# Optimization experiments

Measured on AMD Instinct MI355X. Metric: run time of the kernel, lower is better.

Reference implementation:

```python
import jax, jax.numpy as jnp
import numpy as np

N = 4096      # sentences in document
K = 32        # clusters (args.k)
D = 256       # input_dim
H = 128       # hidden_dim
P_SAL = 0.5   # args.percent_sal


def setup_inputs() -> dict:
    key = jax.random.key(0)
    ks = jax.random.split(key, 12)
    s = 1.0 / np.sqrt(H)
    inp = {
        "sent_gae_embeds": jax.random.normal(ks[0], (N, D), jnp.float32),
        "labels": jax.random.randint(ks[1], (N,), 0, K),
        # GRU layer 0 (torch gate order r,z,n)
        "W_ih0": jax.random.uniform(ks[2], (3 * H, D), jnp.float32, -s, s),
        "W_hh0": jax.random.uniform(ks[3], (3 * H, H), jnp.float32, -s, s),
        "b_ih0": jax.random.uniform(ks[4], (3 * H,), jnp.float32, -s, s),
        "b_hh0": jax.random.uniform(ks[5], (3 * H,), jnp.float32, -s, s),
        # GRU layer 1
        "W_ih1": jax.random.uniform(ks[6], (3 * H, H), jnp.float32, -s, s),
        "W_hh1": jax.random.uniform(ks[7], (3 * H, H), jnp.float32, -s, s),
        "b_ih1": jax.random.uniform(ks[8], (3 * H,), jnp.float32, -s, s),
        "b_hh1": jax.random.uniform(ks[9], (3 * H,), jnp.float32, -s, s),
        # weight-normed linear: W = g * v / ||v|| (norm over input dim)
        "lin_v": jax.random.normal(ks[10], (1, D + H), jnp.float32) * 0.05,
        "lin_g": jnp.ones((1, 1), jnp.float32),
        "lin_b": jnp.zeros((1,), jnp.float32),
    }
    return inp


def _gru_layer(x, W_ih, W_hh, b_ih, b_hh):
    # x: [T, B, Din] -> outputs [T, B, H]
    xw = jnp.einsum("tbd,gd->tbg", x, W_ih) + b_ih  # precompute input gates

    def step(h, xw_t):
        hw = h @ W_hh.T + b_hh
        r = jax.nn.sigmoid(xw_t[:, :H] + hw[:, :H])
        z = jax.nn.sigmoid(xw_t[:, H:2 * H] + hw[:, H:2 * H])
        n = jnp.tanh(xw_t[:, 2 * H:] + r * hw[:, 2 * H:])
        h_new = (1.0 - z) * n + z * h
        return h_new, h_new

    h0 = jnp.zeros((x.shape[1], H), x.dtype)
    _, outs = jax.lax.scan(step, h0, xw)
    return outs


def reference(sent_gae_embeds, labels, W_ih0, W_hh0, b_ih0, b_hh0,
              W_ih1, W_hh1, b_ih1, b_hh1, lin_v, lin_g, lin_b):
    # --- cluster gather: position of each sentence within its cluster ---
    onehot = jax.nn.one_hot(labels, K, dtype=jnp.int32)          # [N, K]
    pos = jnp.cumsum(onehot, axis=0)[jnp.arange(N), labels] - 1  # [N]
    lengths = onehot.sum(axis=0)                                 # [K]

    # padded per-cluster sequences: [T=N, B=K, D]
    padded = jnp.zeros((N, K, D), sent_gae_embeds.dtype).at[pos, labels].set(sent_gae_embeds)

    # --- 2-layer GRU over each cluster sequence ---
    h1 = _gru_layer(padded, W_ih0, W_hh0, b_ih0, b_hh0)
    h2 = _gru_layer(h1, W_ih1, W_hh1, b_ih1, b_hh1)
    len_c = jnp.maximum(lengths, 1)  # empty cluster -> length-1 zero sequence
    cluster_embeds = h2[len_c - 1, jnp.arange(K)]  # [K, H]

    # --- scatter cluster embeds back onto sentences (sent detached as in torch) ---
    sent_d = jax.lax.stop_gradient(sent_gae_embeds)
    final_embeds = jnp.concatenate([sent_d, cluster_embeds[labels]], axis=-1)  # [N, D+H]

    # weight-normed linear + tanh
    Wn = lin_g * lin_v / jnp.linalg.norm(lin_v, axis=1, keepdims=True)
    scores = jnp.tanh(final_embeds @ Wn.T + lin_b)[:, 0]  # [N]

    # salience: per-cluster segment-sum normalization
    clu_scores = jax.ops.segment_sum(scores, labels, num_segments=K)
    sal_scores = scores / clu_scores[labels]

    # position scores: max(0.5, exp(-(i+1)/n**(1/3)))
    inv = np.float32(1.0 / (N ** (1.0 / 3.0)))
    pos_scores = jnp.maximum(0.5, jnp.exp(-(jnp.arange(N, dtype=jnp.float32) + 1.0) * inv))

    return P_SAL * sal_scores + (1.0 - P_SAL) * pos_scores
```

## Files before the change

### kernel.cpp

```cpp
#include <hip/hip_runtime.h>
#include <cmath>

#define NN 4096
#define KK 32
#define DD 256
#define HH 128
#define G3 384
#define CH 16
#define RH 136

typedef __attribute__((ext_vector_type(8))) _Float16 h8;
typedef __attribute__((ext_vector_type(4))) float f32x4;

__global__ __launch_bounds__(1024) void setup_k(
    const int* __restrict__ labels, const float* __restrict__ lin_v,
    const float* __restrict__ lin_g,
    const float* __restrict__ Whh0, const float* __restrict__ Wih1,
    const float* __restrict__ Whh1,
    int* __restrict__ order, int* __restrict__ pos, int* __restrict__ len,
    int* __restrict__ starts, float* __restrict__ scale,
    _Float16* __restrict__ P) {
  if (blockIdx.x != 0) {
    const int gid = (int)(blockIdx.x - 1) * 1024 + threadIdx.x;
    if (gid >= 18432) return;
    const int lane = gid & 63;
    const int kt = (gid >> 6) & 3;
    const int nt = (gid >> 8) % 24;
    const int mat = (gid >> 8) / 24;
    const float* W = (mat == 0) ? Whh0 : (mat == 1 ? Wih1 : Whh1);
    const int n = nt * 16 + (lane & 15);
    const int kbase = kt * 32 + (lane >> 4) * 8;
    _Float16* dst = P + (size_t)gid * 8;
#pragma unroll
    for (int j = 0; j < 8; ++j) dst[j] = (_Float16)W[(size_t)n * HH + kbase + j];
    return;
  }
  const int t = threadIdx.x;
  const int wv = t >> 6, lane = t & 63;
  __shared__ int lens_s[KK];
  for (int cc = 0; cc < 2; ++cc) {
    const int c = wv * 2 + cc;
    int count = 0;
    for (int base = 0; base < NN; base += 64) {
      const int i = base + lane;
      const bool f = (labels[i] == c);
      const unsigned long long m = __ballot(f);
      if (f) {
        const int p = count + __popcll(m & ((1ull << lane) - 1ull));
        order[c * NN + p] = i;
        pos[i] = p;
      }
      count += __popcll(m);
    }
    if (lane == 0) { lens_s[c] = count; len[c] = count; }
  }
  __syncthreads();
  if (wv == 0) {
    int lm = 0;
    if (lane < KK) { const int l = lens_s[lane]; lm = (l > 0) ? l : 1; }
    int inc = lm;
    for (int off = 1; off < KK; off <<= 1) {
      const int o = __shfl_up(inc, off);
      if (lane >= off) inc += o;
    }
    if (lane < KK) starts[lane] = inc - lm;
    if (lane == KK - 1) starts[KK] = inc;
  } else if (wv == 1) {
    float s = 0.f;
    for (int j = lane; j < G3; j += 64) { const float v = lin_v[j]; s += v * v; }
    for (int off = 32; off; off >>= 1) s += __shfl_down(s, off);
    if (lane == 0) scale[0] = lin_g[0] / sqrtf(s);
  }
}

__global__ __launch_bounds__(256) void gemm_ih_k(
    const float* __restrict__ X, const float* __restrict__ W,
    const float* __restrict__ bias,
    const int* __restrict__ labels, const int* __restrict__ pos,
    const int* __restrict__ starts, float* __restrict__ out) {
  __shared__ float Xs[16][132];
  __shared__ float Ws[16][68];
  const int i0 = blockIdx.x * 128;
  const int g0 = blockIdx.y * 64;
  const int t  = threadIdx.x;
  const int it = t & 15;
  const int gt = t >> 4;
  float acc[8][4] = {};
  for (int k0 = 0; k0 < DD; k0 += 16) {
#pragma unroll
    for (int l = 0; l < 2; ++l) {
      const int u = t * 2 + l;
      const int r = u >> 2;
      const int cq = u & 3;
      const float4 f = *(const float4*)(X + (size_t)(i0 + r) * DD + k0 + cq * 4);
      Xs[cq * 4 + 0][r] = f.x; Xs[cq * 4 + 1][r] = f.y;
      Xs[cq * 4 + 2][r] = f.z; Xs[cq * 4 + 3][r] = f.w;
    }
    {
      const int r = t >> 2;
      const int cq = t & 3;
      const float4 f = *(const float4*)(W + (size_t)(g0 + r) * DD + k0 + cq * 4);
      Ws[cq * 4 + 0][r] = f.x; Ws[cq * 4 + 1][r] = f.y;
      Ws[cq * 4 + 2][r] = f.z; Ws[cq * 4 + 3][r] = f.w;
    }
    __syncthreads();
#pragma unroll
    for (int k = 0; k < 16; ++k) {
      float a[8], b[4];
#pragma unroll
      for (int x = 0; x < 8; ++x) a[x] = Xs[k][it * 8 + x];
#pragma unroll
      for (int y = 0; y < 4; ++y) b[y] = Ws[k][gt * 4 + y];
#pragma unroll
      for (int x = 0; x < 8; ++x)
#pragma unroll
        for (int y = 0; y < 4; ++y)
          acc[x][y] += a[x] * b[y];
    }
    __syncthreads();
  }
  const float4 bs = *(const float4*)(bias + g0 + gt * 4);
#pragma unroll
  for (int x = 0; x < 8; ++x) {
    const int gi = i0 + it * 8 + x;
    const int slot = starts[labels[gi]] + pos[gi];
    float4 o;
    o.x = acc[x][0] + bs.x; o.y = acc[x][1] + bs.y;
    o.z = acc[x][2] + bs.z; o.w = acc[x][3] + bs.w;
    *(float4*)(out + (size_t)slot * G3 + g0 + gt * 4) = o;
  }
}

__global__ __launch_bounds__(768) void gru_fused_k(
    const float* __restrict__ xw0,
    const _Float16* __restrict__ pack,
    const float* __restrict__ b_hh0, const float* __restrict__ b_ih0,
    const float* __restrict__ b_ih1, const float* __restrict__ b_hh1,
    const int* __restrict__ starts, const int* __restrict__ len,
    const int* __restrict__ order, const float* __restrict__ sent,
    const float* __restrict__ lin_v, const float* __restrict__ scale,
    const float* __restrict__ lin_b, float* __restrict__ out) {
  const int c = blockIdx.x;
  const int t = threadIdx.x;
  const int wv = t >> 6, lane = t & 63;
  const int group = wv >> 2;
  const int v = wv & 3;
  h8 B[6][4];
  {
    const _Float16* mp = pack + (size_t)group * (24 * 4 * 64 * 8);
#pragma unroll
    for (int i = 0; i < 6; ++i) {
      const int nt = (i >> 1) * 8 + 2 * v + (i & 1);
#pragma unroll
      for (int kt = 0; kt < 4; ++kt)
        B[i][kt] = *(const h8*)(mp + ((size_t)(nt * 4 + kt) * 64 + lane) * 8);
    }
  }
  const int L = len[c], start = starts[c];
  const int Lr = (L > 0) ? L : 1;
  const bool use_bih0 = (L == 0);
  __shared__ __align__(16) float xwbuf[2 * CH * G3];
  __shared__ __align__(16) _Float16 ring[16][2 * RH];
  __shared__ __align__(16) _Float16 hp2[2][2][HH];
  __shared__ float xw1buf[2][8][G3];
  __shared__ float ce_s[HH];
  __shared__ float vbuf[G3];
  __shared__ float sc_s[2048];
  __shared__ float sc_red;
  {
    _Float16* rp = &ring[0][0];
    for (int u = t; u < 16 * 2 * RH; u += 768) rp[u] = (_Float16)0.f;
  }
  if (t < HH) {
    hp2[0][0][t] = (_Float16)0.f; hp2[0][1][t] = (_Float16)0.f;
    hp2[1][0][t] = (_Float16)0.f; hp2[1][1][t] = (_Float16)0.f;
  }
  if (!use_bih0) {
    const float4* src = (const float4*)(xw0 + (size_t)start * G3);
    float4* dst = (float4*)xwbuf;
    dst[t] = src[t];
    dst[t + 768] = src[t + 768];
  }
  const int tg = 32 * v + (lane & 31);
  float bhr = 0.f, bhz = 0.f, bhn = 0.f;
  float bir = 0.f, biz = 0.f, bin = 0.f;
  float h = 0.f;
  if (lane < 32) {
    if (group == 0) {
      bhr = b_hh0[tg]; bhz = b_hh0[HH + tg]; bhn = b_hh0[2 * HH + tg];
      if (use_bih0) {
        bir = b_ih0[tg]; biz = b_ih0[HH + tg]; bin = b_ih0[2 * HH + tg];
      }
    } else if (group == 2) {
      bhr = b_hh1[tg]; bhz = b_hh1[HH + tg]; bhn = b_hh1[2 * HH + tg];
      bir = b_ih1[tg]; biz = b_ih1[HH + tg]; bin = b_ih1[2 * HH + tg];
    }
  }
  __syncthreads();
  const int q = lane >> 4;
  const int row = lane & 15;
  const int hs = (row == 0 || row == 4) ? 0 : 1;
  const bool hiacc = ((lane >> 4) & 1) != 0;
  for (int it2 = 0; it2 < Lr + 9; ++it2) {
    const int par = it2 & 1;
    if (!use_bih0 && (it2 & (CH - 1)) == 0 && it2 + CH < Lr) {
      const float4* src = (const float4*)(xw0 + (size_t)(start + it2 + CH) * G3);
      float4* dst = (float4*)(xwbuf + ((((it2 >> 4) + 1) & 1) ? CH * G3 : 0));
      dst[t] = src[t];
      dst[t + 768] = src[t + 768];
    }
    if (group == 0) {
      if (it2 < Lr) {
        float xr = bir, xz = biz, xn = bin;
        if (!use_bih0 && lane < 32) {
          const float* xrow = xwbuf + ((it2 >> 4) & 1) * (CH * G3)
                                    + (it2 & (CH - 1)) * G3;
          xr = xrow[tg]; xz = xrow[HH + tg]; xn = xrow[2 * HH + tg];
        }
        const _Float16* abse = &ring[(it2 - 1) & 15][hs * RH];
        h8 A[4];
#pragma unroll
        for (int kt = 0; kt < 4; ++kt)
          A[kt] = *(const h8*)(abse + kt * 32 + q * 8);
        f32x4 a0[6];
#pragma unroll
        for (int i = 0; i < 6; ++i) {
          f32x4 a = {0.f, 0.f, 0.f, 0.f};
#pragma unroll
          for (int kt = 0; kt < 4; ++kt)
            a = __builtin_amdgcn_mfma_f32_16x16x32_f16(A[kt], B[i][kt], a, 0, 0, 0);
          a0[i] = a;
        }
        if (lane < 32) {
          const float hwrA = a0[0][0] + a0[0][1], hwrB = a0[1][0] + a0[1][1];
          const float hwzA = a0[2][0] + a0[2][1], hwzB = a0[3][0] + a0[3][1];
          const float hwnA = a0[4][0] + a0[4][1], hwnB = a0[5][0] + a0[5][1];
          const float hwr = hiacc ? hwrB : hwrA;
          const float hwz = hiacc ? hwzB : hwzA;
          const float hwn = hiacc ? hwnB : hwnA;
          const float r = 1.f / (1.f + __expf(-(xr + bhr + hwr)));
          const float z = 1.f / (1.f + __expf(-(xz + bhz + hwz)));
          float tgt = xn + r * (bhn + hwn);
          tgt = fminf(fmaxf(tgt, -15.f), 15.f);
          const float e = __expf(2.f * tgt);
          const float n = (e - 1.f) / (e + 1.f);
          h = (1.f - z) * n + z * h;
          const _Float16 hi = (_Float16)h;
          _Float16* rs = &ring[it2 & 15][0];
          rs[tg] = hi;  rs[RH + tg] = (_Float16)(h - (float)hi);
        }
      }
    } else if (group == 1) {
      if (it2 >= 8 && (it2 & 7) == 0 && it2 - 8 < Lr) {
        const int c8 = it2 - 8;
        const int m = lane & 15;
        const int s = m >> 1, half = m & 1;
        const _Float16* abse = &ring[(c8 + s) & 15][half * RH];
        h8 A[4];
#pragma unroll
        for (int kt = 0; kt < 4; ++kt)
          A[kt] = *(const h8*)(abse + kt * 32 + q * 8);
        const int cbuf = (c8 >> 3) & 1;
        float* xo0 = &xw1buf[cbuf][2 * q][0];
        float* xo1 = &xw1buf[cbuf][2 * q + 1][0];
#pragma unroll
        for (int i = 0; i < 6; ++i) {
          f32x4 a = {0.f, 0.f, 0.f, 0.f};
#pragma unroll
          for (int kt = 0; kt < 4; ++kt)
            a = __builtin_amdgcn_mfma_f32_16x16x32_f16(A[kt], B[i][kt], a, 0, 0, 0);
          const int nt = (i >> 1) * 8 + 2 * v + (i & 1);
          const int col = nt * 16 + (lane & 15);
          xo0[col] = a[0] + a[1];
          xo1[col] = a[2] + a[3];
        }
      }
    } else {
      if (it2 >= 9) {
        const int j = it2 - 9;
        float xr = 0.f, xz = 0.f, xn = 0.f;
        if (lane < 32) {
          const float* xi = xw1buf[(j >> 3) & 1][j & 7];
          xr = xi[tg] + bir; xz = xi[HH + tg] + biz; xn = xi[2 * HH + tg] + bin;
        }
        const _Float16* hbase = hp2[par][hs];
        h8 A[4];
#pragma unroll
        for (int kt = 0; kt < 4; ++kt)
          A[kt] = *(const h8*)(hbase + kt * 32 + q * 8);
        f32x4 a1[6];
#pragma unroll
        for (int i = 0; i < 6; ++i) {
          f32x4 a = {0.f, 0.f, 0.f, 0.f};
#pragma unroll
          for (int kt = 0; kt < 4; ++kt)
            a = __builtin_amdgcn_mfma_f32_16x16x32_f16(A[kt], B[i][kt], a, 0, 0, 0);
          a1[i] = a;
        }
        if (lane < 32) {
          const float hwrA = a1[0][0] + a1[0][1], hwrB = a1[1][0] + a1[1][1];
          const float hwzA = a1[2][0] + a1[2][1], hwzB = a1[3][0] + a1[3][1];
          const float hwnA = a1[4][0] + a1[4][1], hwnB = a1[5][0] + a1[5][1];
          const float hwr = hiacc ? hwrB : hwrA;
          const float hwz = hiacc ? hwzB : hwzA;
          const float hwn = hiacc ? hwnB : hwnA;
          const float r = 1.f / (1.f + __expf(-(xr + bhr + hwr)));
          const float z = 1.f / (1.f + __expf(-(xz + bhz + hwz)));
          float tgt = xn + r * (bhn + hwn);
          tgt = fminf(fmaxf(tgt, -15.f), 15.f);
          const float e = __expf(2.f * tgt);
          const float n = (e - 1.f) / (e + 1.f);
          h = (1.f - z) * n + z * h;
          const _Float16 hi = (_Float16)h;
          hp2[par ^ 1][0][tg] = hi;
          hp2[par ^ 1][1][tg] = (_Float16)(h - (float)hi);
        }
      }
    }
    __syncthreads();
  }
  if (L == 0) return;
  if (group == 2 && lane < 32) ce_s[tg] = h;
  if (t < G3) vbuf[t] = lin_v[t];
  __syncthreads();
  if (wv == 0) {
    float cd = ce_s[lane] * vbuf[DD + lane] + ce_s[64 + lane] * vbuf[DD + 64 + lane];
    for (int off = 32; off; off >>= 1) cd += __shfl_down(cd, off);
    if (lane == 0) sc_red = cd;
  }
  __syncthreads();
  const float cedot = sc_red;
  const float sc = scale[0], lb = lin_b[0];
  const int Lc = (L < 2048) ? L : 2048;
  for (int p = wv; p < Lc; p += 12) {
    const int i = order[c * NN + p];
    const float4 a = *(const float4*)(sent + (size_t)i * DD + lane * 4);
    const float4 b = ((const float4*)vbuf)[lane];
    float d = a.x * b.x + a.y * b.y + a.z * b.z + a.w * b.w;
    for (int off = 32; off; off >>= 1) d += __shfl_down(d, off);
    if (lane == 0) sc_s[p] = tanhf(sc * (d + cedot) + lb);
  }
  __syncthreads();
  if (wv == 0) {
    float s = 0.f;
    for (int p = lane; p < Lc; p += 64) s += sc_s[p];
    for (int off = 32; off; off >>= 1) s += __shfl_down(s, off);
    if (lane == 0) sc_red = 1.f / s;
  }
  __syncthreads();
  const float inv = sc_red;
  for (int p = t; p < Lc; p += 768) {
    const int i = order[c * NN + p];
    float ps = __expf(-(float)(i + 1) * 0.0625f);
    ps = fmaxf(0.5f, ps);
    out[i] = 0.5f * (sc_s[p] * inv) + 0.5f * ps;
  }
}

extern "C" void kernel_launch(void* const* d_in, const int* in_sizes, int n_in,
                              void* d_out, int out_size, void* d_ws, size_t ws_size,
                              hipStream_t stream) {
  const float* sent   = (const float*)d_in[0];
  const int*   labels = (const int*)d_in[1];
  const float* W_ih0  = (const float*)d_in[2];
  const float* W_hh0  = (const float*)d_in[3];
  const float* b_ih0  = (const float*)d_in[4];
  const float* b_hh0  = (const float*)d_in[5];
  const float* W_ih1  = (const float*)d_in[6];
  const float* W_hh1  = (const float*)d_in[7];
  const float* b_ih1  = (const float*)d_in[8];
  const float* b_hh1  = (const float*)d_in[9];
  const float* lin_v  = (const float*)d_in[10];
  const float* lin_g  = (const float*)d_in[11];
  const float* lin_b  = (const float*)d_in[12];
  float* out = (float*)d_out;

  char* ws = (char*)d_ws;
  size_t off = 0;
  auto alloc = [&](size_t bytes) -> void* {
    void* p = ws + off;
    off = (off + bytes + 255) & ~(size_t)255;
    return p;
  };
  int*   order  = (int*)  alloc((size_t)KK * NN * sizeof(int));
  int*   pos    = (int*)  alloc(NN * sizeof(int));
  int*   len    = (int*)  alloc(KK * sizeof(int));
  int*   starts = (int*)  alloc((KK + 1) * sizeof(int));
  float* scale  = (float*)alloc(sizeof(float));
  _Float16* pack = (_Float16*)alloc((size_t)18432 * 8 * sizeof(_Float16));
  float* xw     = (float*)alloc((size_t)(NN + KK + 2 * CH) * G3 * sizeof(float));
  (void)ws_size; (void)in_sizes; (void)n_in; (void)out_size;

  setup_k<<<dim3(19), dim3(1024), 0, stream>>>(
      labels, lin_v, lin_g, W_hh0, W_ih1, W_hh1,
      order, pos, len, starts, scale, pack);
  gemm_ih_k<<<dim3(32, 6), dim3(256), 0, stream>>>(
      sent, W_ih0, b_ih0, labels, pos, starts, xw);
  gru_fused_k<<<dim3(KK), dim3(768), 0, stream>>>(
      xw, pack, b_hh0, b_ih0, b_ih1, b_hh1, starts, len,
      order, sent, lin_v, scale, lin_b, out);
}
```

Baseline: 277.9 us.

## Merge setup and input-GEMM kernels, gather xw rows by order in GRU kernel

Folds the label bucketing, weight packing, norm scale and input-gate GEMM into one launch. The GEMM no longer depends on the per-cluster prefix sums, so it writes rows in sentence order, and the GRU kernel gathers each cluster's rows through the order index when refilling its shared buffer. This removes a kernel launch and the serial dependency on the starts/pos computation. In exchange, the GRU prefetch now does scattered, index-dependent row loads instead of contiguous ones.

```diff
diff --git a/kernel.cpp b/kernel.cpp
--- a/kernel.cpp
+++ b/kernel.cpp
@@ -12,17 +12,19 @@
 typedef __attribute__((ext_vector_type(8))) _Float16 h8;
 typedef __attribute__((ext_vector_type(4))) float f32x4;
 
-__global__ __launch_bounds__(1024) void setup_k(
+__global__ __launch_bounds__(256) void prep_k(
     const int* __restrict__ labels, const float* __restrict__ lin_v,
     const float* __restrict__ lin_g,
     const float* __restrict__ Whh0, const float* __restrict__ Wih1,
     const float* __restrict__ Whh1,
-    int* __restrict__ order, int* __restrict__ pos, int* __restrict__ len,
-    int* __restrict__ starts, float* __restrict__ scale,
-    _Float16* __restrict__ P) {
-  if (blockIdx.x != 0) {
-    const int gid = (int)(blockIdx.x - 1) * 1024 + threadIdx.x;
-    if (gid >= 18432) return;
+    const float* __restrict__ sent, const float* __restrict__ W_ih0,
+    const float* __restrict__ b_ih0,
+    int* __restrict__ order, int* __restrict__ len, float* __restrict__ scale,
+    _Float16* __restrict__ P, float* __restrict__ xw) {
+  const int blk = blockIdx.x;
+  const int t = threadIdx.x;
+  if (blk < 72) {
+    const int gid = blk * 256 + t;
     const int lane = gid & 63;
     const int kt = (gid >> 6) & 3;
     const int nt = (gid >> 8) % 24;
@@ -35,54 +37,34 @@
     for (int j = 0; j < 8; ++j) dst[j] = (_Float16)W[(size_t)n * HH + kbase + j];
     return;
   }
-  const int t = threadIdx.x;
-  const int wv = t >> 6, lane = t & 63;
-  __shared__ int lens_s[KK];
-  for (int cc = 0; cc < 2; ++cc) {
-    const int c = wv * 2 + cc;
+  if (blk < 80) {
+    const int wv = t >> 6, lane = t & 63;
+    const int c = (blk - 72) * 4 + wv;
     int count = 0;
     for (int base = 0; base < NN; base += 64) {
       const int i = base + lane;
       const bool f = (labels[i] == c);
       const unsigned long long m = __ballot(f);
-      if (f) {
-        const int p = count + __popcll(m & ((1ull << lane) - 1ull));
-        order[c * NN + p] = i;
-        pos[i] = p;
-      }
+      if (f) order[c * NN + count + __popcll(m & ((1ull << lane) - 1ull))] = i;
       count += __popcll(m);
     }
-    if (lane == 0) { lens_s[c] = count; len[c] = count; }
-  }
-  __syncthreads();
-  if (wv == 0) {
-    int lm = 0;
-    if (lane < KK) { const int l = lens_s[lane]; lm = (l > 0) ? l : 1; }
-    int inc = lm;
-    for (int off = 1; off < KK; off <<= 1) {
-      const int o = __shfl_up(inc, off);
-      if (lane >= off) inc += o;
-    }
-    if (lane < KK) starts[lane] = inc - lm;
-    if (lane == KK - 1) starts[KK] = inc;
-  } else if (wv == 1) {
-    float s = 0.f;
-    for (int j = lane; j < G3; j += 64) { const float v = lin_v[j]; s += v * v; }
-    for (int off = 32; off; off >>= 1) s += __shfl_down(s, off);
-    if (lane == 0) scale[0] = lin_g[0] / sqrtf(s);
-  }
-}
-
-__global__ __launch_bounds__(256) void gemm_ih_k(
-    const float* __restrict__ X, const float* __restrict__ W,
-    const float* __restrict__ bias,
-    const int* __restrict__ labels, const int* __restrict__ pos,
-    const int* __restrict__ starts, float* __restrict__ out) {
+    if (lane == 0) len[c] = count;
+    return;
+  }
+  if (blk == 80) {
+    if (t < 64) {
+      float s = 0.f;
+      for (int j = t; j < G3; j += 64) { const float v = lin_v[j]; s += v * v; }
+      for (int off = 32; off; off >>= 1) s += __shfl_down(s, off);
+      if (t == 0) scale[0] = lin_g[0] / sqrtf(s);
+    }
+    return;
+  }
   __shared__ float Xs[16][132];
   __shared__ float Ws[16][68];
-  const int i0 = blockIdx.x * 128;
-  const int g0 = blockIdx.y * 64;
-  const int t  = threadIdx.x;
+  const int g = blk - 81;
+  const int i0 = (g & 31) * 128;
+  const int g0 = (g >> 5) * 64;
   const int it = t & 15;
   const int gt = t >> 4;
   float acc[8][4] = {};
@@ -92,14 +74,14 @@
       const int u = t * 2 + l;
       const int r = u >> 2;
       const int cq = u & 3;
-      const float4 f = *(const float4*)(X + (size_t)(i0 + r) * DD + k0 + cq * 4);
+      const float4 f = *(const float4*)(sent + (size_t)(i0 + r) * DD + k0 + cq * 4);
       Xs[cq * 4 + 0][r] = f.x; Xs[cq * 4 + 1][r] = f.y;
       Xs[cq * 4 + 2][r] = f.z; Xs[cq * 4 + 3][r] = f.w;
     }
     {
       const int r = t >> 2;
       const int cq = t & 3;
-      const float4 f = *(const float4*)(W + (size_t)(g0 + r) * DD + k0 + cq * 4);
+      const float4 f = *(const float4*)(W_ih0 + (size_t)(g0 + r) * DD + k0 + cq * 4);
       Ws[cq * 4 + 0][r] = f.x; Ws[cq * 4 + 1][r] = f.y;
       Ws[cq * 4 + 2][r] = f.z; Ws[cq * 4 + 3][r] = f.w;
     }
@@ -119,15 +101,14 @@
     }
     __syncthreads();
   }
-  const float4 bs = *(const float4*)(bias + g0 + gt * 4);
+  const float4 bs = *(const float4*)(b_ih0 + g0 + gt * 4);
 #pragma unroll
   for (int x = 0; x < 8; ++x) {
     const int gi = i0 + it * 8 + x;
-    const int slot = starts[labels[gi]] + pos[gi];
     float4 o;
     o.x = acc[x][0] + bs.x; o.y = acc[x][1] + bs.y;
     o.z = acc[x][2] + bs.z; o.w = acc[x][3] + bs.w;
-    *(float4*)(out + (size_t)slot * G3 + g0 + gt * 4) = o;
+    *(float4*)(xw + (size_t)gi * G3 + g0 + gt * 4) = o;
   }
 }
 
@@ -136,8 +117,8 @@
     const _Float16* __restrict__ pack,
     const float* __restrict__ b_hh0, const float* __restrict__ b_ih0,
     const float* __restrict__ b_ih1, const float* __restrict__ b_hh1,
-    const int* __restrict__ starts, const int* __restrict__ len,
-    const int* __restrict__ order, const float* __restrict__ sent,
+    const int* __restrict__ len, const int* __restrict__ order,
+    const float* __restrict__ sent,
     const float* __restrict__ lin_v, const float* __restrict__ scale,
     const float* __restrict__ lin_b, float* __restrict__ out) {
   const int c = blockIdx.x;
@@ -156,9 +137,11 @@
         B[i][kt] = *(const h8*)(mp + ((size_t)(nt * 4 + kt) * 64 + lane) * 8);
     }
   }
-  const int L = len[c], start = starts[c];
+  const int L = len[c];
   const int Lr = (L > 0) ? L : 1;
   const bool use_bih0 = (L == 0);
+  const int u0 = t / 96, f0 = t - u0 * 96;
+  const int u1 = (t + 768) / 96, f1 = (t + 768) - u1 * 96;
   __shared__ __align__(16) float xwbuf[2 * CH * G3];
   __shared__ __align__(16) _Float16 ring[16][2 * RH];
   __shared__ __align__(16) _Float16 hp2[2][2][HH];
@@ -176,10 +159,12 @@
     hp2[1][0][t] = (_Float16)0.f; hp2[1][1][t] = (_Float16)0.f;
   }
   if (!use_bih0) {
-    const float4* src = (const float4*)(xw0 + (size_t)start * G3);
+    const float4* src = (const float4*)xw0;
     float4* dst = (float4*)xwbuf;
-    dst[t] = src[t];
-    dst[t + 768] = src[t + 768];
+    const int r0 = (u0 < L) ? order[c * NN + u0] : 0;
+    const int r1 = (u1 < L) ? order[c * NN + u1] : 0;
+    dst[t] = src[(size_t)r0 * 96 + f0];
+    dst[t + 768] = src[(size_t)r1 * 96 + f1];
   }
   const int tg = 32 * v + (lane & 31);
   float bhr = 0.f, bhz = 0.f, bhn = 0.f;
@@ -204,10 +189,14 @@
   for (int it2 = 0; it2 < Lr + 9; ++it2) {
     const int par = it2 & 1;
     if (!use_bih0 && (it2 & (CH - 1)) == 0 && it2 + CH < Lr) {
-      const float4* src = (const float4*)(xw0 + (size_t)(start + it2 + CH) * G3);
+      const float4* src = (const float4*)xw0;
       float4* dst = (float4*)(xwbuf + ((((it2 >> 4) + 1) & 1) ? CH * G3 : 0));
-      dst[t] = src[t];
-      dst[t + 768] = src[t + 768];
+      const int p0 = it2 + CH + u0;
+      const int p1 = it2 + CH + u1;
+      const int r0 = (p0 < L) ? order[c * NN + p0] : 0;
+      const int r1 = (p1 < L) ? order[c * NN + p1] : 0;
+      dst[t] = src[(size_t)r0 * 96 + f0];
+      dst[t + 768] = src[(size_t)r1 * 96 + f1];
     }
     if (group == 0) {
       if (it2 < Lr) {
@@ -383,20 +372,16 @@
     return p;
   };
   int*   order  = (int*)  alloc((size_t)KK * NN * sizeof(int));
-  int*   pos    = (int*)  alloc(NN * sizeof(int));
   int*   len    = (int*)  alloc(KK * sizeof(int));
-  int*   starts = (int*)  alloc((KK + 1) * sizeof(int));
   float* scale  = (float*)alloc(sizeof(float));
   _Float16* pack = (_Float16*)alloc((size_t)18432 * 8 * sizeof(_Float16));
-  float* xw     = (float*)alloc((size_t)(NN + KK + 2 * CH) * G3 * sizeof(float));
+  float* xw     = (float*)alloc((size_t)NN * G3 * sizeof(float));
   (void)ws_size; (void)in_sizes; (void)n_in; (void)out_size;
 
-  setup_k<<<dim3(19), dim3(1024), 0, stream>>>(
+  prep_k<<<dim3(273), dim3(256), 0, stream>>>(
       labels, lin_v, lin_g, W_hh0, W_ih1, W_hh1,
-      order, pos, len, starts, scale, pack);
-  gemm_ih_k<<<dim3(32, 6), dim3(256), 0, stream>>>(
-      sent, W_ih0, b_ih0, labels, pos, starts, xw);
+      sent, W_ih0, b_ih0, order, len, scale, pack, xw);
   gru_fused_k<<<dim3(KK), dim3(768), 0, stream>>>(
-      xw, pack, b_hh0, b_ih0, b_ih1, b_hh1, starts, len,
-      order, sent, lin_v, scale, lin_b, out);
+      xw, pack, b_hh0, b_ih0, b_ih1, b_hh1, len, order,
+      sent, lin_v, scale, lin_b, out);
 }
```

New measurement: 241.2 us (median of 2 runs). 1.15x faster.
